# Optimization experiments

Measured on AMD Instinct MI355X. Metric: run time of the kernel, lower is better.

Reference implementation:

```python
import jax, jax.numpy as jnp
import numpy as np

HIDDEN = 128
MIN_DIST = 0.01


def setup_inputs() -> dict:
    key = jax.random.key(0)
    ks = jax.random.split(key, 7)
    B, N, D = 4, 1024, 3
    pos_scaled = jax.random.normal(ks[0], (B, N, D), dtype=jnp.float32)
    # PyTorch Linear: y = x @ W.T + b ; store W as (in, out) for clean einsum
    s1 = 1.0 / np.sqrt(3.0)
    s2 = 1.0 / np.sqrt(HIDDEN)
    W1 = jax.random.uniform(ks[1], (3, HIDDEN), jnp.float32, -s1, s1)
    b1 = jax.random.uniform(ks[2], (HIDDEN,), jnp.float32, -s1, s1)
    W2 = jax.random.uniform(ks[3], (HIDDEN, HIDDEN), jnp.float32, -s2, s2)
    b2 = jax.random.uniform(ks[4], (HIDDEN,), jnp.float32, -s2, s2)
    W3 = jax.random.uniform(ks[5], (HIDDEN, 1), jnp.float32, -s2, s2)
    b3 = jax.random.uniform(ks[6], (1,), jnp.float32, -s2, s2)
    return {"pos_scaled": pos_scaled, "W1": W1, "b1": b1, "W2": W2, "b2": b2, "W3": W3, "b3": b3}


def reference(pos_scaled, W1, b1, W2, b2, W3, b3):
    B, N, _ = pos_scaled.shape
    diff = pos_scaled[:, :, None, :] - pos_scaled[:, None, :, :]   # (B,N,N,3)
    dist = jnp.linalg.norm(diff, axis=-1, keepdims=True)           # (B,N,N,1)
    dist_clip = jnp.maximum(dist, MIN_DIST)
    inv_r = 1.0 / dist_clip
    feat = jnp.concatenate([dist, inv_r, inv_r * inv_r], axis=-1)  # (B,N,N,3)
    h = jnp.tanh(feat @ W1 + b1)
    h = jnp.tanh(h @ W2 + b2)
    mag = h @ W3 + b3                                              # (B,N,N,1)
    mask = (~jnp.eye(N, dtype=bool))[None, :, :, None]             # (1,N,N,1)
    pair_forces = jnp.where(mask, mag * (diff / dist_clip), 0.0)
    return jnp.sum(pair_forces, axis=2)                            # (B,N,3)
```

## Files before the change

kernel.cpp:

```cpp
#include <hip/hip_runtime.h>

#define NPTS   1024
#define HID    128
#define K_TAB  2048
#define U0f    (-10.0f)
#define U1f    (4.0f)

__device__ __forceinline__ float fast_exp2(float x) {
#if __has_builtin(__builtin_amdgcn_exp2f)
    return __builtin_amdgcn_exp2f(x);
#else
    return exp2f(x);
#endif
}
__device__ __forceinline__ float fast_rcp(float x) {
#if __has_builtin(__builtin_amdgcn_rcpf)
    return __builtin_amdgcn_rcpf(x);
#else
    return 1.0f / x;
#endif
}
__device__ __forceinline__ float fast_log2(float x) {
#if __has_builtin(__builtin_amdgcn_logf)
    return __builtin_amdgcn_logf(x);
#else
    return __log2f(x);
#endif
}
__device__ __forceinline__ float fast_rsq(float x) {
#if __has_builtin(__builtin_amdgcn_rsqf)
    return __builtin_amdgcn_rsqf(x);
#else
    return rsqrtf(x);
#endif
}
__device__ __forceinline__ float fast_tanh(float x) {
    float e = fast_exp2(2.8853900817779268f * x);
    return 1.0f - 2.0f * fast_rcp(e + 1.0f);
}

__global__ __launch_bounds__(256) void build_table(const float* __restrict__ W1,
                                                   const float* __restrict__ b1,
                                                   const float* __restrict__ W2,
                                                   const float* __restrict__ b2,
                                                   const float* __restrict__ W3,
                                                   const float* __restrict__ b3,
                                                   float* __restrict__ tab)
{
    __shared__ float h1s[8][HID];
    __shared__ float red[8][HID];

    const int t = threadIdx.x, wave = t >> 6, lane = t & 63;
    const float dU  = (U1f - U0f) / (float)K_TAB;
    const float b3v = b3[0];
    const int   e0  = blockIdx.x * 8;

    for (int tau = t; tau < 8 * HID; tau += 256) {
        int ee = tau >> 7, n = tau & 127;
        int e  = e0 + ee; if (e > K_TAB) e = K_TAB;
        float u    = U0f + (float)e * dU;
        float d    = fast_exp2(u);
        float invc = fast_rcp(fmaxf(d, 0.01f));
        float inv2 = invc * invc;
        float z = fmaf(d, W1[n], fmaf(invc, W1[HID + n], fmaf(inv2, W1[2 * HID + n], b1[n])));
        h1s[ee][n] = fast_tanh(z);
    }
    __syncthreads();
    {
        int n = t & 127, eh = (t >> 7) * 4;
        float a0 = b2[n], a1 = a0, a2 = a0, a3 = a0;
#pragma unroll 8
        for (int k = 0; k < HID; ++k) {
            float w = W2[k * HID + n];
            a0 = fmaf(h1s[eh + 0][k], w, a0);
            a1 = fmaf(h1s[eh + 1][k], w, a1);
            a2 = fmaf(h1s[eh + 2][k], w, a2);
            a3 = fmaf(h1s[eh + 3][k], w, a3);
        }
        float w3n = W3[n];
        red[eh + 0][n] = fast_tanh(a0) * w3n;
        red[eh + 1][n] = fast_tanh(a1) * w3n;
        red[eh + 2][n] = fast_tanh(a2) * w3n;
        red[eh + 3][n] = fast_tanh(a3) * w3n;
    }
    __syncthreads();
    for (int ee = wave; ee < 8; ee += 4) {
        float s = red[ee][lane] + red[ee][lane + 64];
#pragma unroll
        for (int off = 1; off < 64; off <<= 1) s += __shfl_xor(s, off);
        if (lane == 0 && e0 + ee <= K_TAB) tab[e0 + ee] = s + b3v;
    }
}

__global__ __launch_bounds__(256) void forces_kernel(const float* __restrict__ pos,
                                                     const float* __restrict__ tab,
                                                     float* __restrict__ out)
{
    __shared__ float tab_s[K_TAB + 4];
    __shared__ float pos_s[NPTS * 3];

    const int t = threadIdx.x, wave = t >> 6, lane = t & 63;
    const int b  = blockIdx.x >> 7;
    const int ig = blockIdx.x & 127;

    for (int idx = t; idx <= K_TAB; idx += 256) tab_s[idx] = tab[idx];
    {
        const float4* gp = (const float4*)(pos + b * NPTS * 3);
        float4* sp = (float4*)pos_s;
        for (int idx = t; idx < NPTS * 3 / 4; idx += 256) sp[idx] = gp[idx];
    }
    __syncthreads();

    const int   ia = ig * 8 + wave;
    const int   ib = ia + 4;
    const float pax = pos_s[ia * 3 + 0], pay = pos_s[ia * 3 + 1], paz = pos_s[ia * 3 + 2];
    const float pbx = pos_s[ib * 3 + 0], pby = pos_s[ib * 3 + 1], pbz = pos_s[ib * 3 + 2];
    const float S = (float)K_TAB / (U1f - U0f);

    float fax = 0.f, fay = 0.f, faz = 0.f;
    float fbx = 0.f, fby = 0.f, fbz = 0.f;
#pragma unroll 4
    for (int j = lane; j < NPTS; j += 64) {
        float qx = pos_s[j * 3 + 0], qy = pos_s[j * 3 + 1], qz = pos_s[j * 3 + 2];

        float dax = pax - qx, day = pay - qy, daz = paz - qz;
        float dbx = pbx - qx, dby = pby - qy, dbz = pbz - qz;
        float r2a = fmaf(dax, dax, fmaf(day, day, daz * daz));
        float r2b = fmaf(dbx, dbx, fmaf(dby, dby, dbz * dbz));

        float ta = fmaf(0.5f * fast_log2(r2a), S, -U0f * S);
        float tb = fmaf(0.5f * fast_log2(r2b), S, -U0f * S);
        float ka = fminf(fmaxf(floorf(ta), 0.0f), (float)(K_TAB - 1));
        float kb = fminf(fmaxf(floorf(tb), 0.0f), (float)(K_TAB - 1));
        float fra = fminf(fmaxf(ta - ka, 0.0f), 1.0f);
        float frb = fminf(fmaxf(tb - kb, 0.0f), 1.0f);
        int ka_i = (int)ka, kb_i = (int)kb;
        float va0 = tab_s[ka_i], va1 = tab_s[ka_i + 1];
        float vb0 = tab_s[kb_i], vb1 = tab_s[kb_i + 1];
        float maga = fmaf(va1 - va0, fra, va0);
        float magb = fmaf(vb1 - vb0, frb, vb0);

        float sa = maga * fminf(fast_rsq(r2a), 100.0f);
        float sb = magb * fminf(fast_rsq(r2b), 100.0f);
        fax = fmaf(sa, dax, fax); fay = fmaf(sa, day, fay); faz = fmaf(sa, daz, faz);
        fbx = fmaf(sb, dbx, fbx); fby = fmaf(sb, dby, fby); fbz = fmaf(sb, dbz, fbz);
    }
#pragma unroll
    for (int off = 1; off < 64; off <<= 1) {
        fax += __shfl_xor(fax, off); fay += __shfl_xor(fay, off); faz += __shfl_xor(faz, off);
        fbx += __shfl_xor(fbx, off); fby += __shfl_xor(fby, off); fbz += __shfl_xor(fbz, off);
    }
    if (lane == 0) {
        int oa = (b * NPTS + ia) * 3;
        int ob = (b * NPTS + ib) * 3;
        out[oa + 0] = fax; out[oa + 1] = fay; out[oa + 2] = faz;
        out[ob + 0] = fbx; out[ob + 1] = fby; out[ob + 2] = fbz;
    }
}

extern "C" void kernel_launch(void* const* d_in, const int* in_sizes, int n_in,
                              void* d_out, int out_size, void* d_ws, size_t ws_size,
                              hipStream_t stream) {
    const float* pos = (const float*)d_in[0];
    const float* W1  = (const float*)d_in[1];
    const float* b1  = (const float*)d_in[2];
    const float* W2  = (const float*)d_in[3];
    const float* b2  = (const float*)d_in[4];
    const float* W3  = (const float*)d_in[5];
    const float* b3  = (const float*)d_in[6];
    float* out  = (float*)d_out;
    float* tab  = (float*)d_ws;

    int B = (in_sizes[0] / 3) / NPTS;
    build_table<<<K_TAB / 8 + 1, 256, 0, stream>>>(W1, b1, W2, b2, W3, b3, tab);
    forces_kernel<<<B * 128, 256, 0, stream>>>(pos, tab, out);
}
```

Baseline: 79.20 us.

## Fuse table build into forces kernel using bf16 MFMA, smaller table

Merges the two kernels into one launch. Each block now rebuilds a smaller 512-entry lookup table itself, running the second MLP layer in bf16 MFMA from shared memory. The blocks grow to 512 threads with 16 points each. This removes the second launch and the global round trip for the table. In exchange every block repeats the table construction, and the coarser table plus bf16 weights lower accuracy.

```diff
diff --git a/kernel.cpp b/kernel.cpp
--- a/kernel.cpp
+++ b/kernel.cpp
@@ -1,10 +1,17 @@
 #include <hip/hip_runtime.h>
+#include <hip/hip_bf16.h>
 
 #define NPTS   1024
 #define HID    128
-#define K_TAB  2048
+#define K_TAB  512
+#define NPASS  5
 #define U0f    (-10.0f)
 #define U1f    (4.0f)
+#define LDH    136
+
+typedef __bf16 bf16_t;
+typedef __bf16 bf16x8 __attribute__((ext_vector_type(8)));
+typedef float  f32x4  __attribute__((ext_vector_type(4)));
 
 __device__ __forceinline__ float fast_exp2(float x) {
 #if __has_builtin(__builtin_amdgcn_exp2f)
@@ -39,83 +46,115 @@
     return 1.0f - 2.0f * fast_rcp(e + 1.0f);
 }
 
-__global__ __launch_bounds__(256) void build_table(const float* __restrict__ W1,
-                                                   const float* __restrict__ b1,
-                                                   const float* __restrict__ W2,
-                                                   const float* __restrict__ b2,
-                                                   const float* __restrict__ W3,
-                                                   const float* __restrict__ b3,
-                                                   float* __restrict__ tab)
+__launch_bounds__(512, 2)
+__global__ void discovery_one(const float* __restrict__ pos,
+                              const float* __restrict__ W1,
+                              const float* __restrict__ b1,
+                              const float* __restrict__ W2,
+                              const float* __restrict__ b2,
+                              const float* __restrict__ W3,
+                              const float* __restrict__ b3,
+                              float* __restrict__ out)
 {
-    __shared__ float h1s[8][HID];
-    __shared__ float red[8][HID];
-
-    const int t = threadIdx.x, wave = t >> 6, lane = t & 63;
+    __shared__ __align__(16) bf16_t sW[HID * LDH];
+    __shared__ __align__(16) float  tab_s[NPASS * 128];
+    __shared__ float  pos_s[NPTS * 3];
+    __shared__ f32x4  w1s[HID];
+    __shared__ float  b2s[HID];
+    __shared__ float  w3s[HID];
+
+    const int t    = threadIdx.x;
+    const int wave = t >> 6;
+    const int lane = t & 63;
+    const int ln   = lane & 15;
+    const int q    = lane >> 4;
+
+    const int b  = blockIdx.x >> 6;
+    const int ig = blockIdx.x & 63;
+
+    {
+        const float4* gp = (const float4*)(pos + b * NPTS * 3);
+        float4* sp = (float4*)pos_s;
+        for (int idx = t; idx < NPTS * 3 / 4; idx += 512) sp[idx] = gp[idx];
+    }
+    if (t < HID) {
+        f32x4 w = { W1[t], W1[HID + t], W1[2 * HID + t], b1[t] };
+        w1s[t] = w;
+        b2s[t] = b2[t];
+        w3s[t] = W3[t];
+    }
+    for (int idx = t; idx < HID * HID; idx += 512) {
+        int k = idx >> 7, n = idx & 127;
+        sW[n * LDH + k] = (bf16_t)W2[idx];
+    }
+    __syncthreads();
+
+    bf16x8 wfrag[8][4];
+#pragma unroll
+    for (int nt = 0; nt < 8; ++nt)
+#pragma unroll
+        for (int ks = 0; ks < 4; ++ks)
+            wfrag[nt][ks] = *(const bf16x8*)&sW[(nt * 16 + ln) * LDH + ks * 32 + q * 8];
+
     const float dU  = (U1f - U0f) / (float)K_TAB;
     const float b3v = b3[0];
-    const int   e0  = blockIdx.x * 8;
-
-    for (int tau = t; tau < 8 * HID; tau += 256) {
-        int ee = tau >> 7, n = tau & 127;
-        int e  = e0 + ee; if (e > K_TAB) e = K_TAB;
-        float u    = U0f + (float)e * dU;
+
+    for (int p = 0; p < NPASS; ++p) {
+        const int base = p * 128 + wave * 16;
+        int   ec   = base + ln; if (ec > K_TAB) ec = K_TAB;
+        float u    = U0f + (float)ec * dU;
         float d    = fast_exp2(u);
         float invc = fast_rcp(fmaxf(d, 0.01f));
         float inv2 = invc * invc;
-        float z = fmaf(d, W1[n], fmaf(invc, W1[HID + n], fmaf(inv2, W1[2 * HID + n], b1[n])));
-        h1s[ee][n] = fast_tanh(z);
+
+        bf16x8 afr[4];
+#pragma unroll
+        for (int ks = 0; ks < 4; ++ks) {
+#pragma unroll
+            for (int j = 0; j < 8; ++j) {
+                f32x4 w = w1s[ks * 32 + q * 8 + j];
+                float z = fmaf(d, w[0], fmaf(invc, w[1], fmaf(inv2, w[2], w[3])));
+                afr[ks][j] = (bf16_t)fast_tanh(z);
+            }
+        }
+
+        f32x4 zero = { 0.f, 0.f, 0.f, 0.f };
+        f32x4 acc[8];
+#pragma unroll
+        for (int nt = 0; nt < 8; ++nt) acc[nt] = zero;
+#pragma unroll
+        for (int ks = 0; ks < 4; ++ks)
+#pragma unroll
+            for (int nt = 0; nt < 8; ++nt)
+                acc[nt] = __builtin_amdgcn_mfma_f32_16x16x32_bf16(afr[ks], wfrag[nt][ks], acc[nt], 0, 0, 0);
+
+        float pm[4] = {0.f, 0.f, 0.f, 0.f};
+#pragma unroll
+        for (int nt = 0; nt < 8; ++nt) {
+            float b2n = b2s[nt * 16 + ln];
+            float w3n = w3s[nt * 16 + ln];
+#pragma unroll
+            for (int r = 0; r < 4; ++r)
+                pm[r] += fast_tanh(acc[nt][r] + b2n) * w3n;
+        }
+#pragma unroll
+        for (int off = 1; off < 16; off <<= 1)
+#pragma unroll
+            for (int r = 0; r < 4; ++r)
+                pm[r] += __shfl_xor(pm[r], off);
+        if (ln == 0) {
+            f32x4 v = { pm[0] + b3v, pm[1] + b3v, pm[2] + b3v, pm[3] + b3v };
+            *(f32x4*)&tab_s[base + q * 4] = v;
+        }
     }
     __syncthreads();
-    {
-        int n = t & 127, eh = (t >> 7) * 4;
-        float a0 = b2[n], a1 = a0, a2 = a0, a3 = a0;
-#pragma unroll 8
-        for (int k = 0; k < HID; ++k) {
-            float w = W2[k * HID + n];
-            a0 = fmaf(h1s[eh + 0][k], w, a0);
-            a1 = fmaf(h1s[eh + 1][k], w, a1);
-            a2 = fmaf(h1s[eh + 2][k], w, a2);
-            a3 = fmaf(h1s[eh + 3][k], w, a3);
-        }
-        float w3n = W3[n];
-        red[eh + 0][n] = fast_tanh(a0) * w3n;
-        red[eh + 1][n] = fast_tanh(a1) * w3n;
-        red[eh + 2][n] = fast_tanh(a2) * w3n;
-        red[eh + 3][n] = fast_tanh(a3) * w3n;
-    }
-    __syncthreads();
-    for (int ee = wave; ee < 8; ee += 4) {
-        float s = red[ee][lane] + red[ee][lane + 64];
-#pragma unroll
-        for (int off = 1; off < 64; off <<= 1) s += __shfl_xor(s, off);
-        if (lane == 0 && e0 + ee <= K_TAB) tab[e0 + ee] = s + b3v;
-    }
-}
-
-__global__ __launch_bounds__(256) void forces_kernel(const float* __restrict__ pos,
-                                                     const float* __restrict__ tab,
-                                                     float* __restrict__ out)
-{
-    __shared__ float tab_s[K_TAB + 4];
-    __shared__ float pos_s[NPTS * 3];
-
-    const int t = threadIdx.x, wave = t >> 6, lane = t & 63;
-    const int b  = blockIdx.x >> 7;
-    const int ig = blockIdx.x & 127;
-
-    for (int idx = t; idx <= K_TAB; idx += 256) tab_s[idx] = tab[idx];
-    {
-        const float4* gp = (const float4*)(pos + b * NPTS * 3);
-        float4* sp = (float4*)pos_s;
-        for (int idx = t; idx < NPTS * 3 / 4; idx += 256) sp[idx] = gp[idx];
-    }
-    __syncthreads();
-
-    const int   ia = ig * 8 + wave;
-    const int   ib = ia + 4;
+
+    const float S  = (float)K_TAB / (U1f - U0f);
+    const int   ia = ig * 16 + wave * 2;
+    const int   ib = ia + 1;
+
     const float pax = pos_s[ia * 3 + 0], pay = pos_s[ia * 3 + 1], paz = pos_s[ia * 3 + 2];
     const float pbx = pos_s[ib * 3 + 0], pby = pos_s[ib * 3 + 1], pbz = pos_s[ib * 3 + 2];
-    const float S = (float)K_TAB / (U1f - U0f);
 
     float fax = 0.f, fay = 0.f, faz = 0.f;
     float fbx = 0.f, fby = 0.f, fbz = 0.f;
@@ -168,10 +207,8 @@
     const float* b2  = (const float*)d_in[4];
     const float* W3  = (const float*)d_in[5];
     const float* b3  = (const float*)d_in[6];
-    float* out  = (float*)d_out;
-    float* tab  = (float*)d_ws;
+    float* out = (float*)d_out;
 
     int B = (in_sizes[0] / 3) / NPTS;
-    build_table<<<K_TAB / 8 + 1, 256, 0, stream>>>(W1, b1, W2, b2, W3, b3, tab);
-    forces_kernel<<<B * 128, 256, 0, stream>>>(pos, tab, out);
-}
+    discovery_one<<<B * 64, 512, 0, stream>>>(pos, W1, b1, W2, b2, W3, b3, out);
+}
```

Measured after the change: 110.7 us. 39.7% more time.
